# Kernel optimization log

Hardware: AMD Instinct MI355X
Metric: run time of the kernel (lower is better)

Reference implementation:

```python
import jax, jax.numpy as jnp
import numpy as np

T = 0.4       # gumbel temperature (self.T)
BASE = 3.0    # sigmoid offset (self.base)
LN_EPS = 1e-5


def setup_inputs() -> dict:
    key = jax.random.key(0)
    ks = jax.random.split(key, 4)
    B, S, D = 2, 2048, 4096
    E, EMB, M = 64, 128, 11008
    return {
        "x": jax.random.normal(ks[0], (B, S, D), dtype=jnp.float32),
        "rnn_state": jax.random.normal(ks[1], (E, EMB), dtype=jnp.float32),
        "Wr": jax.random.normal(ks[2], (E, D), dtype=jnp.float32) * 0.02,
        "Wd": jax.random.normal(ks[3], (M, EMB), dtype=jnp.float32) * 0.02,
        "ln_w": jnp.ones((EMB,), dtype=jnp.float32),
        "ln_b": jnp.zeros((EMB,), dtype=jnp.float32),
    }


def _layernorm(h, w, b):
    mu = jnp.mean(h, axis=-1, keepdims=True)
    var = jnp.var(h, axis=-1, keepdims=True)
    return (h - mu) * jax.lax.rsqrt(var + LN_EPS) * w + b


def reference(x, rnn_state, Wr, Wd, ln_w, ln_b):
    key = jax.random.key(42)
    k1, k2 = jax.random.split(key)
    # router logits: [B, S, E]
    logits = jnp.einsum("bsd,ed->bse", x, Wr)
    # ST gumbel-softmax (hard one-hot routing)
    eps = 1e-20
    u = jax.random.uniform(k1, logits.shape, dtype=logits.dtype)
    g = -jnp.log(-jnp.log(u + eps) + eps)
    y_soft = jax.nn.softmax((logits + g) / T, axis=-1)
    y_hard = jax.nn.one_hot(jnp.argmax(y_soft, axis=-1), logits.shape[-1], dtype=y_soft.dtype)
    router = jax.lax.stop_gradient(y_hard - y_soft) + y_soft
    # gather routed embedding: [B, S, EMB]
    routed = jnp.einsum("bse,ec->bsc", router, rnn_state)
    # LN + GELU (exact erf) + decode: [B, S, M]
    h = jax.nn.gelu(_layernorm(routed, ln_w, ln_b), approximate=False)
    pre = jnp.einsum("bsc,mc->bsm", h, Wd)
    # ST gumbel-sigmoid with offset, hard round
    e = jax.random.exponential(k2, pre.shape, dtype=pre.dtype)
    gum = -jnp.log(e)
    b_soft = jax.nn.sigmoid((pre + gum + BASE) / T)
    b_hard = jnp.round(b_soft)
    binary = jax.lax.stop_gradient(b_hard - b_soft) + b_soft
    return (binary, router)
```

## Files before the change

kernel.cpp:

```cpp
#include <hip/hip_runtime.h>
#include <hip/hip_bf16.h>
#include <stdint.h>

typedef float floatx4 __attribute__((ext_vector_type(4)));

__host__ __device__ inline uint32_t rotl32(uint32_t x, int r) {
#ifdef __HIP_DEVICE_COMPILE__
  return __builtin_amdgcn_alignbit(x, x, 32 - r);
#else
  return (x << r) | (x >> (32 - r));
#endif
}

__host__ __device__ inline void tf2x32(uint32_t k0, uint32_t k1,
                                       uint32_t x0, uint32_t x1,
                                       uint32_t& o0, uint32_t& o1) {
  const uint32_t k2 = k0 ^ k1 ^ 0x1BD11BDAu;
  x0 += k0; x1 += k1;
#define TFR(r) { x0 += x1; x1 = rotl32(x1, r); x1 ^= x0; }
  TFR(13) TFR(15) TFR(26) TFR(6)
  x0 += k1; x1 += k2 + 1u;
  TFR(17) TFR(29) TFR(16) TFR(24)
  x0 += k2; x1 += k0 + 2u;
  TFR(13) TFR(15) TFR(26) TFR(6)
  x0 += k0; x1 += k1 + 3u;
  TFR(17) TFR(29) TFR(16) TFR(24)
  x0 += k1; x1 += k2 + 4u;
  TFR(13) TFR(15) TFR(26) TFR(6)
  x0 += k2; x1 += k0 + 5u;
#undef TFR
  o0 = x0; o1 = x1;
}

__device__ inline uint32_t jax_bits32(uint32_t kA, uint32_t kB, uint32_t i) {
  uint32_t o0, o1;
  tf2x32(kA, kB, 0u, i, o0, o1);
  return o0 ^ o1;
}

__device__ inline float jax_uniform(uint32_t bits) {
  return __uint_as_float((bits >> 9) | 0x3f800000u) - 1.0f;
}

#define D_DIM   4096
#define E_DIM   64
#define EMB     128
#define M_DIM   11008
#define NROWS   4096
#define BIN_N   45088768
#define KSPLIT  32
#define CK      32
#define XSTR    284
#define WSTR    68
#define C2BLKS  172

__device__ inline int qspread(int v) { return v + ((v >> 5) << 2); }

__global__ __launch_bounds__(256) void krnA(const float* __restrict__ x,
                                            const float* __restrict__ Wr,
                                            float* __restrict__ part) {
  __shared__ __align__(16) float xsT[CK * XSTR];
  __shared__ __align__(16) float wsT[CK * WSTR];
  const int rb = blockIdx.x, ks = blockIdx.y, t = threadIdx.x;
  const int rbase = rb * 256, kbase0 = ks * 128;
  const int w = t >> 6, l = t & 63;
  const int xoff = 4 * l + ((l >> 3) << 2);
  const int woff = (w * 16) + ((w * 16 >> 5) << 2);
  float acc[4][16] = {};

  for (int c = 0; c < 4; ++c) {
    const int kbase = kbase0 + c * CK;
#pragma unroll
    for (int it = 0; it < 8; ++it) {
      int idx = t + it * 256;
      int row = idx >> 3, kq = idx & 7;
      float4 v = *(const float4*)&x[(size_t)(rbase + row) * D_DIM + kbase + kq * 4];
      int adr = qspread(row);
      xsT[(kq * 4 + 0) * XSTR + adr] = v.x;
      xsT[(kq * 4 + 1) * XSTR + adr] = v.y;
      xsT[(kq * 4 + 2) * XSTR + adr] = v.z;
      xsT[(kq * 4 + 3) * XSTR + adr] = v.w;
    }
#pragma unroll
    for (int it = 0; it < 2; ++it) {
      int idx = t + it * 256;
      int e = idx >> 3, kq = idx & 7;
      float4 v = *(const float4*)&Wr[(size_t)e * D_DIM + kbase + kq * 4];
      int adr = qspread(e);
      wsT[(kq * 4 + 0) * WSTR + adr] = v.x;
      wsT[(kq * 4 + 1) * WSTR + adr] = v.y;
      wsT[(kq * 4 + 2) * WSTR + adr] = v.z;
      wsT[(kq * 4 + 3) * WSTR + adr] = v.w;
    }
    __syncthreads();
#pragma unroll
    for (int k = 0; k < CK; ++k) {
      const float* xp = &xsT[k * XSTR + xoff];
      const float* wp = &wsT[k * WSTR + woff];
      floatx4 xa = *(const floatx4*)xp;
      floatx4 w0 = *(const floatx4*)(wp);
      floatx4 w1 = *(const floatx4*)(wp + 4);
      floatx4 w2 = *(const floatx4*)(wp + 8);
      floatx4 w3 = *(const floatx4*)(wp + 12);
#pragma unroll
      for (int r = 0; r < 4; ++r) {
#pragma unroll
        for (int e = 0; e < 4; ++e) {
          acc[r][e]      += xa[r] * w0[e];
          acc[r][e + 4]  += xa[r] * w1[e];
          acc[r][e + 8]  += xa[r] * w2[e];
          acc[r][e + 12] += xa[r] * w3[e];
        }
      }
    }
    __syncthreads();
  }
#pragma unroll
  for (int r = 0; r < 4; ++r) {
    float* pp = part + ((size_t)(rbase + 4 * l + r) * KSPLIT + ks) * E_DIM + w * 16;
    *(float4*)(pp + 0)  = make_float4(acc[r][0],  acc[r][1],  acc[r][2],  acc[r][3]);
    *(float4*)(pp + 4)  = make_float4(acc[r][4],  acc[r][5],  acc[r][6],  acc[r][7]);
    *(float4*)(pp + 8)  = make_float4(acc[r][8],  acc[r][9],  acc[r][10], acc[r][11]);
    *(float4*)(pp + 12) = make_float4(acc[r][12], acc[r][13], acc[r][14], acc[r][15]);
  }
}

__global__ __launch_bounds__(256) void krnC2(const float* __restrict__ rnn,
                                             const float* __restrict__ lnw,
                                             const float* __restrict__ lnb,
                                             const float* __restrict__ Wd,
                                             float* __restrict__ P,
                                             float* __restrict__ pminLoc) {
  __shared__ float4 hs[64][33];
  __shared__ float rmin[4];
  const int t = threadIdx.x;
  {
    const int r = t >> 2, q = t & 3;
    const float4* rp = (const float4*)(rnn + r * EMB) + q * 8;
    float4 v[8];
    float s = 0.0f;
#pragma unroll
    for (int j = 0; j < 8; ++j) {
      v[j] = rp[j];
      s += v[j].x + v[j].y + v[j].z + v[j].w;
    }
    s += __shfl_xor(s, 1); s += __shfl_xor(s, 2);
    const float mu = s * (1.0f / 128.0f);
    float qs = 0.0f;
#pragma unroll
    for (int j = 0; j < 8; ++j) {
      float dx = v[j].x - mu, dy = v[j].y - mu, dz = v[j].z - mu, dw = v[j].w - mu;
      qs += dx * dx + dy * dy + dz * dz + dw * dw;
    }
    qs += __shfl_xor(qs, 1); qs += __shfl_xor(qs, 2);
    const float rs = rsqrtf(qs * (1.0f / 128.0f) + 1e-5f);
    const float4* wp = (const float4*)lnw + q * 8;
    const float4* bp = (const float4*)lnb + q * 8;
#pragma unroll
    for (int j = 0; j < 8; ++j) {
      float4 w = wp[j], b = bp[j], g;
      float h;
      h = (v[j].x - mu) * rs * w.x + b.x;
      g.x = 0.5f * h * (1.0f + erff(h * 0.70710678118654752f));
      h = (v[j].y - mu) * rs * w.y + b.y;
      g.y = 0.5f * h * (1.0f + erff(h * 0.70710678118654752f));
      h = (v[j].z - mu) * rs * w.z + b.z;
      g.z = 0.5f * h * (1.0f + erff(h * 0.70710678118654752f));
      h = (v[j].w - mu) * rs * w.w + b.w;
      g.w = 0.5f * h * (1.0f + erff(h * 0.70710678118654752f));
      hs[r][q * 8 + j] = g;
    }
  }
  __syncthreads();
  const int wv = t >> 6, lane = t & 63;
  const int m = blockIdx.x * 64 + lane;
  const float4* wd4 = (const float4*)(Wd + (size_t)m * EMB);
  float acc[16] = {};
  for (int c4 = 0; c4 < 32; ++c4) {
    float4 w = wd4[c4];
#pragma unroll
    for (int e = 0; e < 16; ++e) {
      float4 h = hs[wv * 16 + e][c4];
      acc[e] += w.x * h.x + w.y * h.y + w.z * h.z + w.w * h.w;
    }
  }
  float mn = acc[0];
#pragma unroll
  for (int e = 0; e < 16; ++e) {
    P[(size_t)(wv * 16 + e) * M_DIM + m] = acc[e];
    mn = fminf(mn, acc[e]);
  }
#pragma unroll
  for (int off = 32; off >= 1; off >>= 1)
    mn = fminf(mn, __shfl_xor(mn, off));
  if (lane == 0) rmin[wv] = mn;
  __syncthreads();
  if (t == 0)
    pminLoc[blockIdx.x] = fminf(fminf(rmin[0], rmin[1]), fminf(rmin[2], rmin[3]));
}

__global__ __launch_bounds__(256) void krnB(const float* __restrict__ part,
                                            float* __restrict__ router_out,
                                            int* __restrict__ eidx,
                                            const float* __restrict__ pminLoc,
                                            uint32_t* __restrict__ K9out,
                                            uint32_t K1A, uint32_t K1B) {
  __shared__ float red[4];
  const int t = threadIdx.x;
  const int wv = t >> 6, lane = t & 63;
  const int row = blockIdx.x * 4 + wv;
  float lg = 0.0f;
#pragma unroll
  for (int s = 0; s < KSPLIT; ++s)
    lg += part[((size_t)row * KSPLIT + s) * E_DIM + lane];

  uint32_t jf = (uint32_t)row * 64u + (uint32_t)lane;
  uint32_t bits = jax_bits32(K1A, K1B, jf);
  float u = jax_uniform(bits);
  float inner = -logf(u + 1e-20f);
  float g = -logf(inner + 1e-20f);
  float w = (lg + g) * 2.5f;

  float m = w;
#pragma unroll
  for (int off = 32; off >= 1; off >>= 1) m = fmaxf(m, __shfl_xor(m, off));
  unsigned long long msk = __ballot(w == m);
  int arg = __ffsll(msk) - 1;
  router_out[(size_t)row * E_DIM + lane] = (lane == arg) ? 1.0f : 0.0f;
  if (lane == 0) eidx[row] = arg;

  if (blockIdx.x == 0) {
    float v = (t < C2BLKS) ? pminLoc[t] : 3.0e38f;
#pragma unroll
    for (int off = 32; off >= 1; off >>= 1) v = fminf(v, __shfl_xor(v, off));
    if (lane == 0) red[wv] = v;
    __syncthreads();
    if (t == 0) {
      float pmin = fminf(fminf(red[0], red[1]), fminf(red[2], red[3]));
      float tt = pmin + 2.95f;
      float delta = __expf(-__expf(tt));
      delta = fminf(fmaxf(delta, 1.2e-7f), 0.5f);
      uint32_t Ku = (uint32_t)((1.0f - delta) * 8388608.0f);
      *K9out = Ku << 9;
    }
  }
}

__device__ inline float decide(float pre, uint32_t bits) {
  float u = jax_uniform(bits);
  float om = 1.0f - u;
  float e = -__logf(om);
  float gum = -__logf(e);
  float z = pre + gum + 3.0f;
  return (z > 0.0f) ? 1.0f : 0.0f;
}

__global__ __launch_bounds__(256) void krnD(const float* __restrict__ P,
                                            const int* __restrict__ eidx,
                                            const uint32_t* __restrict__ K9p,
                                            float* __restrict__ out,
                                            uint32_t K2A, uint32_t K2B) {
  const uint32_t K9 = *K9p;

  uint32_t g = (blockIdx.x * 256u + threadIdx.x) * 4u;
  uint32_t b0 = jax_bits32(K2A, K2B, g + 0u);
  uint32_t b1 = jax_bits32(K2A, K2B, g + 1u);
  uint32_t b2 = jax_bits32(K2A, K2B, g + 2u);
  uint32_t b3 = jax_bits32(K2A, K2B, g + 3u);
  floatx4 r = {1.0f, 1.0f, 1.0f, 1.0f};
  uint32_t mx = max(max(b0, b1), max(b2, b3));
  if (mx >= K9) {
    uint32_t row = g / (uint32_t)M_DIM;
    uint32_t m = g - row * (uint32_t)M_DIM;
    const float* pp = &P[(size_t)eidx[row] * M_DIM + m];
    if (b0 >= K9) r.x = decide(pp[0], b0);
    if (b1 >= K9) r.y = decide(pp[1], b1);
    if (b2 >= K9) r.z = decide(pp[2], b2);
    if (b3 >= K9) r.w = decide(pp[3], b3);
  }
  __builtin_nontemporal_store(r, (floatx4*)&out[g]);
}

extern "C" void kernel_launch(void* const* d_in, const int* in_sizes, int n_in,
                              void* d_out, int out_size, void* d_ws, size_t ws_size,
                              hipStream_t stream) {
  const float* x    = (const float*)d_in[0];
  const float* rnn  = (const float*)d_in[1];
  const float* Wr   = (const float*)d_in[2];
  const float* Wd   = (const float*)d_in[3];
  const float* lnw  = (const float*)d_in[4];
  const float* lnb  = (const float*)d_in[5];
  float* out = (float*)d_out;

  uint32_t K1A, K1B, K2A, K2B;
  tf2x32(0u, 42u, 0u, 0u, K1A, K1B);
  tf2x32(0u, 42u, 0u, 1u, K2A, K2B);

  char* ws = (char*)d_ws;
  int*      eidx    = (int*)ws;
  float*    P       = (float*)(ws + 65536);
  float*    pminLoc = (float*)(ws + 2990080);
  uint32_t* K9u     = (uint32_t*)(ws + 2991104);

  float* part = out;
  float* router_out = out + (size_t)BIN_N;

  krnA<<<dim3(16, KSPLIT), 256, 0, stream>>>(x, Wr, part);
  krnC2<<<C2BLKS, 256, 0, stream>>>(rnn, lnw, lnb, Wd, P, pminLoc);
  krnB<<<1024, 256, 0, stream>>>(part, router_out, eidx, pminLoc, K9u, K1A, K1B);
  krnD<<<44032, 256, 0, stream>>>(P, eidx, K9u, out, K2A, K2B);
}
```

Before: 325.8 us.

## Merge router GEMM and decode-GEMM kernels into one launch, stage partial-sum stores through LDS

Combines the router logits split-K kernel and the LN/GELU/decode kernel into a single launch, where the first blocks do the decode work and the rest do the router GEMM. The two independent workloads can then run concurrently and one launch gap is removed. The router partial-sum output is also transposed through shared memory in two halves so global stores become contiguous float4 rows. This costs extra syncthreads and shared-memory traffic, and the shared buffer size now has to fit both roles.

```diff
diff --git a/kernel.cpp b/kernel.cpp
--- a/kernel.cpp
+++ b/kernel.cpp
@@ -53,15 +53,95 @@
 #define XSTR    284
 #define WSTR    68
 #define C2BLKS  172
+#define TSTR    67
 
 __device__ inline int qspread(int v) { return v + ((v >> 5) << 2); }
 
-__global__ __launch_bounds__(256) void krnA(const float* __restrict__ x,
-                                            const float* __restrict__ Wr,
-                                            float* __restrict__ part) {
-  __shared__ __align__(16) float xsT[CK * XSTR];
-  __shared__ __align__(16) float wsT[CK * WSTR];
-  const int rb = blockIdx.x, ks = blockIdx.y, t = threadIdx.x;
+__global__ __launch_bounds__(256) void krnAC2(const float* __restrict__ x,
+                                              const float* __restrict__ Wr,
+                                              float* __restrict__ part,
+                                              const float* __restrict__ rnn,
+                                              const float* __restrict__ lnw,
+                                              const float* __restrict__ lnb,
+                                              const float* __restrict__ Wd,
+                                              float* __restrict__ P,
+                                              float* __restrict__ pminLoc) {
+  __shared__ __align__(16) float smem[CK * XSTR + CK * WSTR + 4];
+  const int t = threadIdx.x;
+
+  if (blockIdx.x < C2BLKS) {
+    float4 (*hs)[33] = (float4(*)[33])smem;
+    float* rmin = smem + 8448;
+    {
+      const int r = t >> 2, q = t & 3;
+      const float4* rp = (const float4*)(rnn + r * EMB) + q * 8;
+      float4 v[8];
+      float s = 0.0f;
+#pragma unroll
+      for (int j = 0; j < 8; ++j) {
+        v[j] = rp[j];
+        s += v[j].x + v[j].y + v[j].z + v[j].w;
+      }
+      s += __shfl_xor(s, 1); s += __shfl_xor(s, 2);
+      const float mu = s * (1.0f / 128.0f);
+      float qs = 0.0f;
+#pragma unroll
+      for (int j = 0; j < 8; ++j) {
+        float dx = v[j].x - mu, dy = v[j].y - mu, dz = v[j].z - mu, dw = v[j].w - mu;
+        qs += dx * dx + dy * dy + dz * dz + dw * dw;
+      }
+      qs += __shfl_xor(qs, 1); qs += __shfl_xor(qs, 2);
+      const float rs = rsqrtf(qs * (1.0f / 128.0f) + 1e-5f);
+      const float4* wp = (const float4*)lnw + q * 8;
+      const float4* bp = (const float4*)lnb + q * 8;
+#pragma unroll
+      for (int j = 0; j < 8; ++j) {
+        float4 w = wp[j], b = bp[j], g;
+        float h;
+        h = (v[j].x - mu) * rs * w.x + b.x;
+        g.x = 0.5f * h * (1.0f + erff(h * 0.70710678118654752f));
+        h = (v[j].y - mu) * rs * w.y + b.y;
+        g.y = 0.5f * h * (1.0f + erff(h * 0.70710678118654752f));
+        h = (v[j].z - mu) * rs * w.z + b.z;
+        g.z = 0.5f * h * (1.0f + erff(h * 0.70710678118654752f));
+        h = (v[j].w - mu) * rs * w.w + b.w;
+        g.w = 0.5f * h * (1.0f + erff(h * 0.70710678118654752f));
+        hs[r][q * 8 + j] = g;
+      }
+    }
+    __syncthreads();
+    const int wv = t >> 6, lane = t & 63;
+    const int m = blockIdx.x * 64 + lane;
+    const float4* wd4 = (const float4*)(Wd + (size_t)m * EMB);
+    float acc[16] = {};
+    for (int c4 = 0; c4 < 32; ++c4) {
+      float4 w = wd4[c4];
+#pragma unroll
+      for (int e = 0; e < 16; ++e) {
+        float4 h = hs[wv * 16 + e][c4];
+        acc[e] += w.x * h.x + w.y * h.y + w.z * h.z + w.w * h.w;
+      }
+    }
+    float mn = acc[0];
+#pragma unroll
+    for (int e = 0; e < 16; ++e) {
+      P[(size_t)(wv * 16 + e) * M_DIM + m] = acc[e];
+      mn = fminf(mn, acc[e]);
+    }
+#pragma unroll
+    for (int off = 32; off >= 1; off >>= 1)
+      mn = fminf(mn, __shfl_xor(mn, off));
+    if (lane == 0) rmin[wv] = mn;
+    __syncthreads();
+    if (t == 0)
+      pminLoc[blockIdx.x] = fminf(fminf(rmin[0], rmin[1]), fminf(rmin[2], rmin[3]));
+    return;
+  }
+
+  float* xsT = smem;
+  float* wsT = smem + CK * XSTR;
+  const int flat = blockIdx.x - C2BLKS;
+  const int rb = flat & 15, ks = flat >> 4;
   const int rbase = rb * 256, kbase0 = ks * 128;
   const int w = t >> 6, l = t & 63;
   const int xoff = 4 * l + ((l >> 3) << 2);
@@ -115,88 +195,30 @@
     }
     __syncthreads();
   }
-#pragma unroll
-  for (int r = 0; r < 4; ++r) {
-    float* pp = part + ((size_t)(rbase + 4 * l + r) * KSPLIT + ks) * E_DIM + w * 16;
-    *(float4*)(pp + 0)  = make_float4(acc[r][0],  acc[r][1],  acc[r][2],  acc[r][3]);
-    *(float4*)(pp + 4)  = make_float4(acc[r][4],  acc[r][5],  acc[r][6],  acc[r][7]);
-    *(float4*)(pp + 8)  = make_float4(acc[r][8],  acc[r][9],  acc[r][10], acc[r][11]);
-    *(float4*)(pp + 12) = make_float4(acc[r][12], acc[r][13], acc[r][14], acc[r][15]);
-  }
-}
-
-__global__ __launch_bounds__(256) void krnC2(const float* __restrict__ rnn,
-                                             const float* __restrict__ lnw,
-                                             const float* __restrict__ lnb,
-                                             const float* __restrict__ Wd,
-                                             float* __restrict__ P,
-                                             float* __restrict__ pminLoc) {
-  __shared__ float4 hs[64][33];
-  __shared__ float rmin[4];
-  const int t = threadIdx.x;
-  {
-    const int r = t >> 2, q = t & 3;
-    const float4* rp = (const float4*)(rnn + r * EMB) + q * 8;
-    float4 v[8];
-    float s = 0.0f;
-#pragma unroll
-    for (int j = 0; j < 8; ++j) {
-      v[j] = rp[j];
-      s += v[j].x + v[j].y + v[j].z + v[j].w;
-    }
-    s += __shfl_xor(s, 1); s += __shfl_xor(s, 2);
-    const float mu = s * (1.0f / 128.0f);
-    float qs = 0.0f;
-#pragma unroll
-    for (int j = 0; j < 8; ++j) {
-      float dx = v[j].x - mu, dy = v[j].y - mu, dz = v[j].z - mu, dw = v[j].w - mu;
-      qs += dx * dx + dy * dy + dz * dz + dw * dw;
-    }
-    qs += __shfl_xor(qs, 1); qs += __shfl_xor(qs, 2);
-    const float rs = rsqrtf(qs * (1.0f / 128.0f) + 1e-5f);
-    const float4* wp = (const float4*)lnw + q * 8;
-    const float4* bp = (const float4*)lnb + q * 8;
-#pragma unroll
-    for (int j = 0; j < 8; ++j) {
-      float4 w = wp[j], b = bp[j], g;
-      float h;
-      h = (v[j].x - mu) * rs * w.x + b.x;
-      g.x = 0.5f * h * (1.0f + erff(h * 0.70710678118654752f));
-      h = (v[j].y - mu) * rs * w.y + b.y;
-      g.y = 0.5f * h * (1.0f + erff(h * 0.70710678118654752f));
-      h = (v[j].z - mu) * rs * w.z + b.z;
-      g.z = 0.5f * h * (1.0f + erff(h * 0.70710678118654752f));
-      h = (v[j].w - mu) * rs * w.w + b.w;
-      g.w = 0.5f * h * (1.0f + erff(h * 0.70710678118654752f));
-      hs[r][q * 8 + j] = g;
-    }
-  }
-  __syncthreads();
-  const int wv = t >> 6, lane = t & 63;
-  const int m = blockIdx.x * 64 + lane;
-  const float4* wd4 = (const float4*)(Wd + (size_t)m * EMB);
-  float acc[16] = {};
-  for (int c4 = 0; c4 < 32; ++c4) {
-    float4 w = wd4[c4];
-#pragma unroll
-    for (int e = 0; e < 16; ++e) {
-      float4 h = hs[wv * 16 + e][c4];
-      acc[e] += w.x * h.x + w.y * h.y + w.z * h.z + w.w * h.w;
-    }
-  }
-  float mn = acc[0];
-#pragma unroll
-  for (int e = 0; e < 16; ++e) {
-    P[(size_t)(wv * 16 + e) * M_DIM + m] = acc[e];
-    mn = fminf(mn, acc[e]);
-  }
-#pragma unroll
-  for (int off = 32; off >= 1; off >>= 1)
-    mn = fminf(mn, __shfl_xor(mn, off));
-  if (lane == 0) rmin[wv] = mn;
-  __syncthreads();
-  if (t == 0)
-    pminLoc[blockIdx.x] = fminf(fminf(rmin[0], rmin[1]), fminf(rmin[2], rmin[3]));
+
+  float* tr = xsT;
+  for (int half = 0; half < 2; ++half) {
+    __syncthreads();
+    if ((l >> 5) == half) {
+      const int lr = l & 31;
+#pragma unroll
+      for (int r = 0; r < 4; ++r) {
+        float* dst = tr + (lr * 4 + r) * TSTR + w * 16;
+        *(float4*)(dst + 0)  = make_float4(acc[r][0],  acc[r][1],  acc[r][2],  acc[r][3]);
+        *(float4*)(dst + 4)  = make_float4(acc[r][4],  acc[r][5],  acc[r][6],  acc[r][7]);
+        *(float4*)(dst + 8)  = make_float4(acc[r][8],  acc[r][9],  acc[r][10], acc[r][11]);
+        *(float4*)(dst + 12) = make_float4(acc[r][12], acc[r][13], acc[r][14], acc[r][15]);
+      }
+    }
+    __syncthreads();
+#pragma unroll
+    for (int it = 0; it < 8; ++it) {
+      const int lrow = (t >> 4) + it * 16;
+      const int grow = rbase + half * 128 + lrow;
+      float4 v = *(const float4*)(tr + lrow * TSTR + (t & 15) * 4);
+      *(float4*)(part + ((size_t)grow * KSPLIT + ks) * E_DIM + (t & 15) * 4) = v;
+    }
+  }
 }
 
 __global__ __launch_bounds__(256) void krnB(const float* __restrict__ part,
@@ -305,8 +327,7 @@
   float* part = out;
   float* router_out = out + (size_t)BIN_N;
 
-  krnA<<<dim3(16, KSPLIT), 256, 0, stream>>>(x, Wr, part);
-  krnC2<<<C2BLKS, 256, 0, stream>>>(rnn, lnw, lnb, Wd, P, pminLoc);
+  krnAC2<<<C2BLKS + 512, 256, 0, stream>>>(x, Wr, part, rnn, lnw, lnb, Wd, P, pminLoc);
   krnB<<<1024, 256, 0, stream>>>(part, router_out, eidx, pminLoc, K9u, K1A, K1B);
   krnD<<<44032, 256, 0, stream>>>(P, eidx, K9u, out, K2A, K2B);
 }
```

Result: no change. 321.1 us (-1.4%).
